# Optimization experiments

Hardware: AMD Instinct MI355X
Metric: run time of the kernel (lower is better)

## Reference

```python
import jax, jax.numpy as jnp
import numpy as np

EPS = 1e-5

def _layernorm(x):
    mu = jnp.mean(x, axis=-1, keepdims=True)
    var = jnp.mean((x - mu) ** 2, axis=-1, keepdims=True)
    return (x - mu) / jnp.sqrt(var + EPS)

def _mlp_silu_ln(h, w0, b0, w1, b1):
    z = jnp.maximum(h @ w0 + b0, 0.0) @ w1 + b1
    z = z * jax.nn.sigmoid(z)  # SiLU
    return _layernorm(z)

def _scatter_mean(msgs, tgt, n_nodes):
    s = jax.ops.segment_sum(msgs, tgt, num_segments=n_nodes)
    cnt = jax.ops.segment_sum(jnp.ones((msgs.shape[0],), msgs.dtype), tgt, num_segments=n_nodes)
    return jnp.where(cnt[:, None] > 0, s / jnp.maximum(cnt, 1.0)[:, None], 0.0)

def setup_inputs() -> dict:
    key = jax.random.key(0)
    ks = jax.random.split(key, 6)
    N, E, D_IN, D = 100000, 600000, 64, 128
    s = 0.1
    return {
        "x": jax.random.normal(ks[0], (N, D_IN), jnp.float32),
        "edge_index": jax.random.randint(ks[1], (2, E), 0, N, jnp.int64),
        "ie_w0": jax.random.normal(ks[2], (D_IN, D), jnp.float32) * s,
        "ie_b0": jnp.zeros((D,), jnp.float32),
        "ie_w1": jax.random.normal(ks[3], (D, D), jnp.float32) * s,
        "ie_b1": jnp.zeros((D,), jnp.float32),
        "lw0": jax.random.normal(ks[4], (3, D, D), jnp.float32) * s,
        "lb0": jnp.zeros((3, D), jnp.float32),
        "lw1": jax.random.normal(ks[5], (3, D, D), jnp.float32) * s,
        "lb1": jnp.zeros((3, D), jnp.float32),
    }

def reference(x, edge_index, ie_w0, ie_b0, ie_w1, ie_b1, lw0, lb0, lw1, lb1):
    n_nodes = x.shape[0]
    src, tgt = edge_index[0], edge_index[1]
    # initial embedding: MLP(relu) -> SiLU -> LayerNorm
    h = _mlp_silu_ln(x, ie_w0, ie_b0, ie_w1, ie_b1)

    def step(h, params):
        w0, b0, w1, b1 = params
        z = _mlp_silu_ln(h, w0, b0, w1, b1)
        agg = _scatter_mean(z[src], tgt, n_nodes)  # mean aggregation over incoming edges
        return agg + h, None  # residual

    h, _ = jax.lax.scan(step, h, (lw0, lb0, lw1, lb1))
    return h
```

## Files before the change

### kernel.cpp

```cpp
#include <hip/hip_runtime.h>

typedef short short8 __attribute__((ext_vector_type(8)));
typedef float f32x4 __attribute__((ext_vector_type(4)));

union V16 { uint4 u; unsigned short s[8]; short8 v; };

#define CAP 48

__device__ __forceinline__ unsigned short f2bf(float f) {
  unsigned u = __builtin_bit_cast(unsigned, f);
  u += 0x7fffu + ((u >> 16) & 1u);
  return (unsigned short)(u >> 16);
}
__device__ __forceinline__ float bf2f(unsigned short b) {
  unsigned u = ((unsigned)b) << 16;
  return __builtin_bit_cast(float, u);
}
__device__ __forceinline__ unsigned cvtpk(float lo, float hi) {
  unsigned r;
  asm("v_cvt_pk_bf16_f32 %0, %1, %2" : "=v"(r) : "v"(lo), "v"(hi));
  return r;
}

__device__ __forceinline__ void tcast_one(const float* __restrict__ w,
                                          uint4* __restrict__ wf, int K, int idx) {
  int NF64 = (K / 4) * 64;
  int b = idx / NF64;
  int r = idx - b * NF64;
  int f = r >> 6;
  int l = r & 63;
  int KB = K / 32;
  int n0 = f / KB;
  int k0 = f - n0 * KB;
  int n = n0 * 16 + (l & 15);
  int ks = k0 * 32 + (l >> 4) * 8;
  const float* src = w + (size_t)b * K * 128 + (size_t)ks * 128 + n;
  V16 o;
#pragma unroll
  for (int j = 0; j < 8; j++) o.s[j] = f2bf(src[j * 128]);
  wf[idx] = o.u;
}

__global__ __launch_bounds__(512) void prep_kernel(
    const float* __restrict__ ie_w0, uint4* __restrict__ w0f_ie,
    const float* __restrict__ ie_w1, uint4* __restrict__ w1f_ie,
    const float* __restrict__ lw0, uint4* __restrict__ w0f_l,
    const float* __restrict__ lw1, uint4* __restrict__ w1f_l,
    const int* __restrict__ ei, int samples, int* __restrict__ flag) {
  int t = blockIdx.x * 512 + threadIdx.x;
  if (t < 1024) { tcast_one(ie_w0, w0f_ie, 64, t); return; }
  t -= 1024;
  if (t < 2048) { tcast_one(ie_w1, w1f_ie, 128, t); return; }
  t -= 2048;
  if (t < 6144) { tcast_one(lw0, w0f_l, 128, t); return; }
  t -= 6144;
  if (t < 6144) { tcast_one(lw1, w1f_l, 128, t); return; }
  t -= 6144;
  if (t < samples && (t & 1) && ei[t] != 0) atomicOr(flag, 1);
}

__global__ void fill_kernel(const int* __restrict__ ei, const int* __restrict__ flag,
                            int* __restrict__ cursor, int* __restrict__ elist, int E) {
  int e = blockIdx.x * 256 + threadIdx.x;
  if (e >= E) return;
  int f = *flag;
  int s = f ? ei[e] : ei[(size_t)e * 2];
  int t = f ? ei[(size_t)E + e] : ei[((size_t)E + e) * 2];
  int p = atomicAdd(&cursor[t], 1);
  if (p < CAP) elist[t * CAP + p] = s;
}

template <int K, bool INBF>
__device__ __forceinline__ void mlp_body(
    const float* __restrict__ inF, const unsigned short* __restrict__ inB,
    const uint4* __restrict__ w0f, const float* __restrict__ b0,
    const uint4* __restrict__ w1f, const float* __restrict__ b1,
    unsigned short* __restrict__ outB, int N, int ntiles,
    uint4* wl, float* bl, int tid) {
  constexpr int KB = K / 32;
  constexpr int NF0 = KB * 8;
  const int lane = tid & 63, wv = tid >> 6;
  for (int i = tid; i < (NF0 + 32) * 64; i += 512)
    wl[i] = (i < NF0 * 64) ? w0f[i] : w1f[i - NF0 * 64];
  if (tid < 128) { bl[tid] = b0[tid]; bl[128 + tid] = b1[tid]; }
  __syncthreads();

  const int c = lane & 15;
  const int q = lane >> 4;
  const int sA = c + 32 * (q & 1);

  for (int tile = blockIdx.x; tile < ntiles; tile += gridDim.x) {
    const int r = tile * 128 + wv * 16 + c;

    short8 afr[KB];
    if (r < N) {
      if (INBF) {
        const unsigned short* rp = inB + (size_t)r * K + q * 8;
#pragma unroll
        for (int k0 = 0; k0 < KB; k0++)
          afr[k0] = *(const short8*)(rp + k0 * 32);
      } else {
        const float* rp = inF + (size_t)r * K + q * 8;
#pragma unroll
        for (int k0 = 0; k0 < KB; k0++) {
          float4 a = *(const float4*)(rp + k0 * 32);
          float4 b = *(const float4*)(rp + k0 * 32 + 4);
          V16 o;
          o.u.x = cvtpk(a.x, a.y); o.u.y = cvtpk(a.z, a.w);
          o.u.z = cvtpk(b.x, b.y); o.u.w = cvtpk(b.z, b.w);
          afr[k0] = o.v;
        }
      }
    } else {
#pragma unroll
      for (int k0 = 0; k0 < KB; k0++) {
        V16 o; o.u.x = 0; o.u.y = 0; o.u.z = 0; o.u.w = 0; afr[k0] = o.v;
      }
    }

    f32x4 acc[8];
#pragma unroll
    for (int n0 = 0; n0 < 8; n0++) {
      acc[n0] = (f32x4){0.f, 0.f, 0.f, 0.f};
#pragma unroll
      for (int k0 = 0; k0 < KB; k0++) {
        V16 w; w.u = wl[(n0 * KB + k0) * 64 + lane];
        acc[n0] = __builtin_amdgcn_mfma_f32_16x16x32_bf16(w.v, afr[k0], acc[n0], 0, 0, 0);
      }
    }

    unsigned pk[8][2];
#pragma unroll
    for (int n0 = 0; n0 < 8; n0++) {
      f32x4 bb = *(const f32x4*)&bl[n0 * 16 + 4 * q];
      float t0 = acc[n0][0] + bb[0]; t0 = t0 > 0.f ? t0 : 0.f;
      float t1 = acc[n0][1] + bb[1]; t1 = t1 > 0.f ? t1 : 0.f;
      float t2 = acc[n0][2] + bb[2]; t2 = t2 > 0.f ? t2 : 0.f;
      float t3 = acc[n0][3] + bb[3]; t3 = t3 > 0.f ? t3 : 0.f;
      pk[n0][0] = cvtpk(t0, t1);
      pk[n0][1] = cvtpk(t2, t3);
    }

    short8 b2[4];
#pragma unroll
    for (int k0 = 0; k0 < 4; k0++) {
      V16 t;
#pragma unroll
      for (int p = 0; p < 4; p++) {
        int src = sA + 16 * (p >> 1);
        unsigned lo = __shfl(pk[2 * k0][p & 1], src, 64);
        unsigned hi = __shfl(pk[2 * k0 + 1][p & 1], src, 64);
        (&t.u.x)[p] = (q & 2) ? hi : lo;
      }
      b2[k0] = t.v;
    }

    f32x4 z[8];
#pragma unroll
    for (int n0 = 0; n0 < 8; n0++) {
      z[n0] = (f32x4){0.f, 0.f, 0.f, 0.f};
#pragma unroll
      for (int k0 = 0; k0 < 4; k0++) {
        V16 w; w.u = wl[NF0 * 64 + (n0 * 4 + k0) * 64 + lane];
        z[n0] = __builtin_amdgcn_mfma_f32_16x16x32_bf16(w.v, b2[k0], z[n0], 0, 0, 0);
      }
    }

    float sum = 0.f, sq = 0.f;
#pragma unroll
    for (int n0 = 0; n0 < 8; n0++) {
      f32x4 bb = *(const f32x4*)&bl[128 + n0 * 16 + 4 * q];
#pragma unroll
      for (int j = 0; j < 4; j++) {
        float v = z[n0][j] + bb[j];
        float sg = v / (1.f + __expf(-v));
        z[n0][j] = sg;
        sum += sg;
        sq += sg * sg;
      }
    }
    sum += __shfl_xor(sum, 16, 64);
    sum += __shfl_xor(sum, 32, 64);
    sq += __shfl_xor(sq, 16, 64);
    sq += __shfl_xor(sq, 32, 64);
    float mu = sum * (1.f / 128.f);
    float rs = rsqrtf(sq * (1.f / 128.f) - mu * mu + 1e-5f);

    if (r < N) {
#pragma unroll
      for (int n0 = 0; n0 < 8; n0++) {
        float v0 = (z[n0][0] - mu) * rs, v1 = (z[n0][1] - mu) * rs;
        float v2 = (z[n0][2] - mu) * rs, v3 = (z[n0][3] - mu) * rs;
        uint2 st; st.x = cvtpk(v0, v1); st.y = cvtpk(v2, v3);
        *(uint2*)(outB + (size_t)r * 128 + n0 * 16 + 4 * q) = st;
      }
    }
  }
}

__global__ __launch_bounds__(512, 4) void mlp64_kernel(
    const float* __restrict__ x, const uint4* __restrict__ w0f,
    const float* __restrict__ b0, const uint4* __restrict__ w1f,
    const float* __restrict__ b1, unsigned short* __restrict__ hB,
    int N, int ntiles) {
  __shared__ uint4 wl[48 * 64];
  __shared__ float bl[256];
  mlp_body<64, false>(x, nullptr, w0f, b0, w1f, b1, hB, N, ntiles,
                      wl, bl, threadIdx.x);
}

__global__ __launch_bounds__(512, 4) void mlp128_kernel(
    const unsigned short* __restrict__ hB, const uint4* __restrict__ w0f,
    const float* __restrict__ b0, const uint4* __restrict__ w1f,
    const float* __restrict__ b1, unsigned short* __restrict__ outB,
    int N, int ntiles) {
  __shared__ uint4 wl[64 * 64];
  __shared__ float bl[256];
  mlp_body<128, true>(nullptr, hB, w0f, b0, w1f, b1, outB, N, ntiles,
                      wl, bl, threadIdx.x);
}

template <bool LAST>
__global__ __launch_bounds__(256) void gather_kernel(
    const unsigned short* __restrict__ z, const int* __restrict__ elist,
    const int* __restrict__ cursor, unsigned short* __restrict__ hB,
    float* __restrict__ hout, int N) {
  int t = blockIdx.x * 256 + threadIdx.x;
  int g = t >> 4;
  if (g >= N) return;
  int lane = threadIdx.x & 63;
  int gb = lane & 48;
  int sub = lane & 15;
  int c = sub * 8;
  int o = g * CAP;
  int n = cursor[g];
  n = n < CAP ? n : CAP;
  V16 hv;
  hv.u = *(const uint4*)(hB + (size_t)g * 128 + c);
  float acc[8] = {0.f, 0.f, 0.f, 0.f, 0.f, 0.f, 0.f, 0.f};
  for (int base = 0; base < n; base += 16) {
    int m = n - base;
    m = m < 16 ? m : 16;
    int sidx = (sub < m) ? elist[o + base + sub] : 0;
    int i = 0;
    for (; i + 4 <= m; i += 4) {
      int s0 = __shfl(sidx, gb + i, 64);
      int s1 = __shfl(sidx, gb + i + 1, 64);
      int s2 = __shfl(sidx, gb + i + 2, 64);
      int s3 = __shfl(sidx, gb + i + 3, 64);
      V16 v0, v1, v2, v3;
      v0.u = *(const uint4*)(z + (size_t)s0 * 128 + c);
      v1.u = *(const uint4*)(z + (size_t)s1 * 128 + c);
      v2.u = *(const uint4*)(z + (size_t)s2 * 128 + c);
      v3.u = *(const uint4*)(z + (size_t)s3 * 128 + c);
#pragma unroll
      for (int j = 0; j < 8; j++)
        acc[j] += (bf2f(v0.s[j]) + bf2f(v1.s[j])) + (bf2f(v2.s[j]) + bf2f(v3.s[j]));
    }
    for (; i < m; i++) {
      int s0 = __shfl(sidx, gb + i, 64);
      V16 v0;
      v0.u = *(const uint4*)(z + (size_t)s0 * 128 + c);
#pragma unroll
      for (int j = 0; j < 8; j++) acc[j] += bf2f(v0.s[j]);
    }
  }
  float inv = n > 0 ? 1.f / (float)n : 0.f;
  float hv_f[8];
#pragma unroll
  for (int j = 0; j < 8; j++) hv_f[j] = bf2f(hv.s[j]) + acc[j] * inv;
  if (LAST) {
    float* hp = hout + (size_t)g * 128 + c;
    float4 h0, h1;
    h0.x = hv_f[0]; h0.y = hv_f[1]; h0.z = hv_f[2]; h0.w = hv_f[3];
    h1.x = hv_f[4]; h1.y = hv_f[5]; h1.z = hv_f[6]; h1.w = hv_f[7];
    *(float4*)hp = h0;
    *(float4*)(hp + 4) = h1;
  } else {
    V16 st;
    st.u.x = cvtpk(hv_f[0], hv_f[1]);
    st.u.y = cvtpk(hv_f[2], hv_f[3]);
    st.u.z = cvtpk(hv_f[4], hv_f[5]);
    st.u.w = cvtpk(hv_f[6], hv_f[7]);
    *(uint4*)(hB + (size_t)g * 128 + c) = st.u;
  }
}

extern "C" void kernel_launch(void* const* d_in, const int* in_sizes, int n_in,
                              void* d_out, int out_size, void* d_ws, size_t ws_size,
                              hipStream_t stream) {
  const float* x = (const float*)d_in[0];
  const int* ei = (const int*)d_in[1];
  const float* ie_w0 = (const float*)d_in[2];
  const float* ie_b0 = (const float*)d_in[3];
  const float* ie_w1 = (const float*)d_in[4];
  const float* ie_b1 = (const float*)d_in[5];
  const float* lw0 = (const float*)d_in[6];
  const float* lb0 = (const float*)d_in[7];
  const float* lw1 = (const float*)d_in[8];
  const float* lb1 = (const float*)d_in[9];
  const int N = in_sizes[0] / 64;
  const int E = in_sizes[1] / 2;
  float* h = (float*)d_out;

  char* ws = (char*)d_ws;
  size_t off_b = 0;
  auto carve = [&](size_t bytes) { void* p = ws + off_b; off_b = (off_b + bytes + 255) & ~(size_t)255; return p; };
  unsigned short* zbuf = (unsigned short*)carve((size_t)N * 128 * 2);
  unsigned short* hbuf = (unsigned short*)carve((size_t)N * 128 * 2);
  int* elist = (int*)carve((size_t)N * CAP * 4);
  int* flag = (int*)carve(256);
  int* cursor = (int*)carve((size_t)N * 4);
  size_t zspan = (char*)(cursor + N) - (char*)flag;
  uint4* w0f_ie = (uint4*)carve(16 * 64 * 16);
  uint4* w1f_ie = (uint4*)carve(32 * 64 * 16);
  uint4* w0f_l = (uint4*)carve(3 * 32 * 64 * 16);
  uint4* w1f_l = (uint4*)carve(3 * 32 * 64 * 16);

  const int ntiles = (N + 127) / 128;
  const int mgrid = ntiles < 512 ? ntiles : 512;
  int samples = 2 * E < 8192 ? 2 * E : 8192;

  hipMemsetAsync(flag, 0, zspan, stream);
  prep_kernel<<<(15360 + samples + 511) / 512, 512, 0, stream>>>(
      ie_w0, w0f_ie, ie_w1, w1f_ie, lw0, w0f_l, lw1, w1f_l, ei, samples, flag);

  fill_kernel<<<(E + 255) / 256, 256, 0, stream>>>(ei, flag, cursor, elist, E);

  mlp64_kernel<<<mgrid, 512, 0, stream>>>(
      x, w0f_ie, ie_b0, w1f_ie, ie_b1, hbuf, N, ntiles);

  for (int l = 0; l < 3; l++) {
    mlp128_kernel<<<mgrid, 512, 0, stream>>>(
        hbuf, w0f_l + (size_t)l * 32 * 64, lb0 + (size_t)l * 128,
        w1f_l + (size_t)l * 32 * 64, lb1 + (size_t)l * 128, zbuf, N, ntiles);
    if (l < 2)
      gather_kernel<false><<<((size_t)N * 16 + 255) / 256, 256, 0, stream>>>(
          zbuf, elist, cursor, hbuf, nullptr, N);
    else
      gather_kernel<true><<<((size_t)N * 16 + 255) / 256, 256, 0, stream>>>(
          zbuf, elist, cursor, hbuf, h, N);
  }
}
```

Baseline: 300.4 us.

## Prefetch next tile's input rows in registers while computing current tile

Splits the MLP input load into issue/commit phases so that the next tile's activations are loaded from global memory into registers while the current tile's MFMAs and LayerNorm run. The first tile's load is also issued before the weight staging into shared memory and the barrier, hiding that latency too. This costs extra registers (nb/nf buffers), which under launch_bounds(512,4) may cause spills or lower occupancy.

```diff
diff --git a/kernel.cpp b/kernel.cpp
--- a/kernel.cpp
+++ b/kernel.cpp
@@ -80,43 +80,69 @@
   constexpr int KB = K / 32;
   constexpr int NF0 = KB * 8;
   const int lane = tid & 63, wv = tid >> 6;
+  const int c = lane & 15;
+  const int q = lane >> 4;
+  const int sA = c + 32 * (q & 1);
+
+  short8 nb[KB];
+  float4 nf[2 * KB];
+
+  auto issue = [&](int tile) {
+    const int r = tile * 128 + wv * 16 + c;
+    const bool valid = r < N;
+    if (INBF) {
+      const unsigned short* rp = inB + (size_t)r * K + q * 8;
+#pragma unroll
+      for (int k0 = 0; k0 < KB; k0++) {
+        V16 o;
+        if (valid) o.u = *(const uint4*)(rp + k0 * 32);
+        else { o.u.x = 0; o.u.y = 0; o.u.z = 0; o.u.w = 0; }
+        nb[k0] = o.v;
+      }
+    } else {
+      const float* rp = inF + (size_t)r * K + q * 8;
+#pragma unroll
+      for (int k0 = 0; k0 < KB; k0++) {
+        if (valid) {
+          nf[2 * k0] = *(const float4*)(rp + k0 * 32);
+          nf[2 * k0 + 1] = *(const float4*)(rp + k0 * 32 + 4);
+        } else {
+          float4 zz; zz.x = 0.f; zz.y = 0.f; zz.z = 0.f; zz.w = 0.f;
+          nf[2 * k0] = zz; nf[2 * k0 + 1] = zz;
+        }
+      }
+    }
+  };
+  auto commit = [&](short8* afr) {
+    if (INBF) {
+#pragma unroll
+      for (int k0 = 0; k0 < KB; k0++) afr[k0] = nb[k0];
+    } else {
+#pragma unroll
+      for (int k0 = 0; k0 < KB; k0++) {
+        float4 a = nf[2 * k0], b = nf[2 * k0 + 1];
+        V16 o;
+        o.u.x = cvtpk(a.x, a.y); o.u.y = cvtpk(a.z, a.w);
+        o.u.z = cvtpk(b.x, b.y); o.u.w = cvtpk(b.z, b.w);
+        afr[k0] = o.v;
+      }
+    }
+  };
+
+  int tile = blockIdx.x;
+  issue(tile);
+
   for (int i = tid; i < (NF0 + 32) * 64; i += 512)
     wl[i] = (i < NF0 * 64) ? w0f[i] : w1f[i - NF0 * 64];
   if (tid < 128) { bl[tid] = b0[tid]; bl[128 + tid] = b1[tid]; }
   __syncthreads();
 
-  const int c = lane & 15;
-  const int q = lane >> 4;
-  const int sA = c + 32 * (q & 1);
-
-  for (int tile = blockIdx.x; tile < ntiles; tile += gridDim.x) {
+  while (tile < ntiles) {
     const int r = tile * 128 + wv * 16 + c;
-
     short8 afr[KB];
-    if (r < N) {
-      if (INBF) {
-        const unsigned short* rp = inB + (size_t)r * K + q * 8;
-#pragma unroll
-        for (int k0 = 0; k0 < KB; k0++)
-          afr[k0] = *(const short8*)(rp + k0 * 32);
-      } else {
-        const float* rp = inF + (size_t)r * K + q * 8;
-#pragma unroll
-        for (int k0 = 0; k0 < KB; k0++) {
-          float4 a = *(const float4*)(rp + k0 * 32);
-          float4 b = *(const float4*)(rp + k0 * 32 + 4);
-          V16 o;
-          o.u.x = cvtpk(a.x, a.y); o.u.y = cvtpk(a.z, a.w);
-          o.u.z = cvtpk(b.x, b.y); o.u.w = cvtpk(b.z, b.w);
-          afr[k0] = o.v;
-        }
-      }
-    } else {
-#pragma unroll
-      for (int k0 = 0; k0 < KB; k0++) {
-        V16 o; o.u.x = 0; o.u.y = 0; o.u.z = 0; o.u.w = 0; afr[k0] = o.v;
-      }
-    }
+    commit(afr);
+    const int next = tile + gridDim.x;
+    if (next < ntiles) issue(next);
 
     f32x4 acc[8];
 #pragma unroll
@@ -195,6 +221,7 @@
         *(uint2*)(outB + (size_t)r * 128 + n0 * 16 + 4 * q) = st;
       }
     }
+    tile = next;
   }
 }
 
```

Measured after the change: 322.5 us. +7.4%, slower.
